# Kernel optimization log

Hardware: AMD Instinct MI355X
Metric: run time of the kernel (lower is better)

The kernel has to match this reference:

```python
import jax, jax.numpy as jnp
import numpy as np

B, I, H = 8192, 1024, 1024

def setup_inputs() -> dict:
    key = jax.random.key(0)
    ks = jax.random.split(key, 5)
    # xavier-uniform-ish scale for weights
    sW = float(np.sqrt(6.0 / (I + H)))
    sU = float(np.sqrt(6.0 / (H + H)))
    return {
        "x": jax.random.normal(ks[0], (B, I), jnp.float32),
        "h": jax.random.normal(ks[1], (B, H), jnp.float32),
        "c": jax.random.normal(ks[2], (B, H), jnp.float32),
        # gate order along leading axis: 0=i, 1=f, 2=o, 3=c_hat
        "W": jax.random.uniform(ks[3], (4, H, I), jnp.float32, -sW, sW),
        "bW": jnp.zeros((4, H), jnp.float32),
        "U": jax.random.uniform(ks[4], (4, H, H), jnp.float32, -sU, sU),
        "bU": jnp.zeros((4, H), jnp.float32),
    }

def reference(x, h, c, W, bW, U, bU):
    # two batched GEMMs covering all 8 original Linear layers
    gx = jnp.einsum('bi,ghi->gbh', x, W) + bW[:, None, :]   # [4,B,H]
    gh = jnp.einsum('bk,ghk->gbh', h, U) + bU[:, None, :]   # [4,B,H]
    g = gx + gh
    i = jax.nn.sigmoid(g[0])
    f = jax.nn.sigmoid(g[1])
    o = jax.nn.sigmoid(g[2])
    c_hat = jnp.tanh(g[3])
    c_new = f * c + i * c_hat
    h_new = o * jnp.tanh(c_new)
    return (h_new, (h_new, c_new))
```

## Files before the change

kernel.cpp:

```cpp
#include <hip/hip_runtime.h>
#include <hip/hip_bf16.h>

typedef __hip_bfloat16 bf16;
typedef __attribute__((ext_vector_type(8))) short short8;
typedef __attribute__((ext_vector_type(4))) float floatx4;

#define B_DIM 8192
#define H_DIM 1024
#define KSUM 2048
#define BM 128
#define BN 128
#define BK 64
#define KITER 32
#define CEX_STRIDE 68

union BS { bf16 b; short s; };
__device__ __forceinline__ short cvt1(float f) {
  BS u; u.b = __float2bfloat16(f); return u.s;
}
__device__ __forceinline__ short8 cvt8(float4 lo, float4 hi) {
  short8 r;
  r[0] = cvt1(lo.x); r[1] = cvt1(lo.y); r[2] = cvt1(lo.z); r[3] = cvt1(lo.w);
  r[4] = cvt1(hi.x); r[5] = cvt1(hi.y); r[6] = cvt1(hi.z); r[7] = cvt1(hi.w);
  return r;
}

__device__ __forceinline__ void async_ld16(const bf16* g, bf16* lds) {
  __builtin_amdgcn_global_load_lds(
      (const __attribute__((address_space(1))) unsigned int*)g,
      (__attribute__((address_space(3))) unsigned int*)lds,
      16, 0, 0);
}

__global__ __launch_bounds__(256) void cvt_pack(
    const float* __restrict__ x, const float* __restrict__ h,
    const float* __restrict__ W, const float* __restrict__ U,
    bf16* __restrict__ Ac, bf16* __restrict__ Bc) {
  const int blk = blockIdx.x;
  if (blk < 8192) {
    const int idx = blk * 256 + threadIdx.x;
    const long row = idx >> 8;
    const int k0 = (idx & 255) << 3;
    const float* src = (k0 < 1024) ? (x + row * 1024 + k0)
                                   : (h + row * 1024 + (k0 - 1024));
    const float4 lo = *(const float4*)src;
    const float4 hi = *(const float4*)(src + 4);
    *(short8*)(Ac + row * KSUM + k0) = cvt8(lo, hi);
  } else {
    const int idx = (blk - 8192) * 256 + threadIdx.x;
    const long r = idx >> 8;
    const int k0 = (idx & 255) << 3;
    const int g = (int)(r & 3);
    const long hh = r >> 2;
    const long base = (long)g * (H_DIM * H_DIM) + hh * H_DIM;
    const float* src = (k0 < 1024) ? (W + base + k0) : (U + base + (k0 - 1024));
    const float4 lo = *(const float4*)src;
    const float4 hi = *(const float4*)(src + 4);
    *(short8*)(Bc + r * KSUM + k0) = cvt8(lo, hi);
  }
}

__device__ __forceinline__ float sigmoidf_(float v) {
  return 1.0f / (1.0f + __expf(-v));
}
__device__ __forceinline__ float tanhf_(float v) {
  return 1.0f - 2.0f / (__expf(2.0f * v) + 1.0f);
}
__device__ __forceinline__ float getc(const float4& v, int t) {
  return t == 0 ? v.x : t == 1 ? v.y : t == 2 ? v.z : v.w;
}

__global__ __launch_bounds__(256) void gemm_lstm(
    const bf16* __restrict__ Ac, const bf16* __restrict__ Bc,
    const float* __restrict__ cprev_g, const float* __restrict__ bW,
    const float* __restrict__ bU, float* __restrict__ out) {
  __shared__ __align__(16) char smem[65536];
  bf16* const sA0 = (bf16*)smem;
  bf16* const sB0 = (bf16*)(smem + 16384);
  bf16* const sA1 = (bf16*)(smem + 32768);
  bf16* const sB1 = (bf16*)(smem + 49152);
  float* const cex = (float*)smem;

  const int tid  = threadIdx.x;
  const int lane = tid & 63;
  const int wv   = tid >> 6;

  const int blk  = blockIdx.x;
  const int xcd  = blk & 7;
  const int slot = blk >> 3;
  const int mt   = slot & 63;
  const int nt   = (xcd << 2) | (slot >> 6);
  const long m0 = (long)mt * BM;
  const long n0 = (long)nt * BN;

  const int lrow   = lane >> 3;
  const int lchunk = lane & 7;
  const int schunk = lchunk ^ lrow;
  const bf16* aSrc = Ac + (m0 + wv * 8 + lrow) * (long)KSUM + schunk * 8;
  const bf16* bSrc = Bc + (n0 + wv * 8 + lrow) * (long)KSUM + schunk * 8;
  bf16* const dA0 = sA0 + wv * 512;
  bf16* const dB0 = sB0 + wv * 512;
  bf16* const dA1 = sA1 + wv * 512;
  bf16* const dB1 = sB1 + wv * 512;

  const int wm = ((wv >> 1) & 1) << 6;
  const int wn = (wv & 1) << 6;
  const int col16 = lane & 15;
  const int quad  = lane >> 4;
  const int x7    = col16 & 7;

  floatx4 acc[4][4];
#pragma unroll
  for (int i = 0; i < 4; ++i)
#pragma unroll
    for (int j = 0; j < 4; ++j) acc[i][j] = (floatx4){0.f, 0.f, 0.f, 0.f};

#define STAGE(kt, dA, dB)                                                 \
  {                                                                       \
    const long koff_ = (long)(kt) * BK;                                   \
    _Pragma("unroll")                                                     \
    for (int q = 0; q < 4; ++q) {                                         \
      async_ld16(aSrc + koff_ + (long)q * (32 * (long)KSUM), (dA) + q * 2048); \
      async_ld16(bSrc + koff_ + (long)q * (32 * (long)KSUM), (dB) + q * 2048); \
    }                                                                     \
  }

#define COMPUTE(sAp, sBp)                                                 \
  {                                                                       \
    _Pragma("unroll")                                                     \
    for (int s = 0; s < 2; ++s) {                                         \
      const int cp = ((((s << 2) + quad) ^ x7) << 3);                     \
      short8 af[4], bfr[4];                                               \
      _Pragma("unroll")                                                   \
      for (int i = 0; i < 4; ++i) {                                       \
        af[i]  = *(const short8*)&(sAp)[(wm + i * 16 + col16) * 64 + cp]; \
        bfr[i] = *(const short8*)&(sBp)[(wn + i * 16 + col16) * 64 + cp]; \
      }                                                                   \
      _Pragma("unroll")                                                   \
      for (int i = 0; i < 4; ++i)                                         \
        _Pragma("unroll")                                                 \
        for (int j = 0; j < 4; ++j)                                       \
          acc[i][j] = __builtin_amdgcn_mfma_f32_16x16x32_bf16(            \
              af[i], bfr[j], acc[i][j], 0, 0, 0);                         \
    }                                                                     \
  }

  STAGE(0, dA0, dB0);
#pragma unroll 1
  for (int kt = 0; kt < KITER; kt += 2) {
    __syncthreads();
    STAGE(kt + 1, dA1, dB1);
    COMPUTE(sA0, sB0);
    __syncthreads();
    if (kt + 2 < KITER) STAGE(kt + 2, dA0, dB0);
    COMPUTE(sA1, sB1);
  }

  __syncthreads();

  const int rquad = (lane >> 4) << 2;
  const int row16 = lane & 15;
  const int tq    = lane >> 4;
  const long hglob = (n0 >> 2) + (wn >> 2) + tq * 4;

  float4 bsum[4];
#pragma unroll
  for (int g = 0; g < 4; ++g) {
    const float4 a = *(const float4*)(bW + g * H_DIM + hglob);
    const float4 b = *(const float4*)(bU + g * H_DIM + hglob);
    bsum[g] = (float4){a.x + b.x, a.y + b.y, a.z + b.z, a.w + b.w};
  }

  float* wx = cex + wv * (16 * CEX_STRIDE);
  const long BH = (long)B_DIM * H_DIM;

  for (int ig = 0; ig < 4; ++ig) {
#pragma unroll
    for (int j = 0; j < 4; ++j)
#pragma unroll
      for (int r = 0; r < 4; ++r)
        wx[(rquad + r) * CEX_STRIDE + j * 16 + col16] = acc[ig][j][r];

    float4 g4[4];
#pragma unroll
    for (int t = 0; t < 4; ++t)
      g4[t] = *(const float4*)&wx[row16 * CEX_STRIDE + (tq * 4 + t) * 4];

    const long mrow = m0 + wm + ig * 16 + row16;
    const float4 cp4 = *(const float4*)(cprev_g + mrow * H_DIM + hglob);

    float hn[4], cn[4];
#pragma unroll
    for (int t = 0; t < 4; ++t) {
      const float gi = g4[t].x + getc(bsum[0], t);
      const float gf = g4[t].y + getc(bsum[1], t);
      const float go = g4[t].z + getc(bsum[2], t);
      const float gg = g4[t].w + getc(bsum[3], t);
      const float I = sigmoidf_(gi);
      const float F = sigmoidf_(gf);
      const float O = sigmoidf_(go);
      const float G = tanhf_(gg);
      const float cv = F * getc(cp4, t) + I * G;
      hn[t] = O * tanhf_(cv);
      cn[t] = cv;
    }
    const float4 hn4 = {hn[0], hn[1], hn[2], hn[3]};
    const float4 cn4 = {cn[0], cn[1], cn[2], cn[3]};
    const long ob = mrow * H_DIM + hglob;
    *(float4*)(out + ob)          = hn4;
    *(float4*)(out + BH + ob)     = hn4;
    *(float4*)(out + 2 * BH + ob) = cn4;
  }
}

extern "C" void kernel_launch(void* const* d_in, const int* in_sizes, int n_in,
                              void* d_out, int out_size, void* d_ws, size_t ws_size,
                              hipStream_t stream) {
  const float* x  = (const float*)d_in[0];
  const float* h  = (const float*)d_in[1];
  const float* c  = (const float*)d_in[2];
  const float* W  = (const float*)d_in[3];
  const float* bW = (const float*)d_in[4];
  const float* U  = (const float*)d_in[5];
  const float* bU = (const float*)d_in[6];
  float* out = (float*)d_out;

  bf16* Ac = (bf16*)d_ws;
  bf16* Bc = (bf16*)((char*)d_ws + (size_t)33554432);

  cvt_pack<<<12288, 256, 0, stream>>>(x, h, W, U, Ac, Bc);
  gemm_lstm<<<2048, 256, 0, stream>>>(Ac, Bc, c, bW, bU, out);
}
```

Before: 374.7 us.

## Use 256x256 tiles with 8 waves and a 10-slot async LDS ring pipeline

Grows the GEMM tile from 128x128 to 256x256 with 512 threads per block, so each block reuses more of A and B per LDS load. Global-to-LDS loads are issued in half-tile chunks into a 10-slot ring buffer, so several stages stay in flight while MFMAs run. The main loop is split into four quarter phases that interleave LDS reads, prefetches, barriers and MFMA bursts, with setprio raising the priority of the MFMA bursts. The cost is 160 KB of dynamic LDS and many more accumulator registers per wave, which limits occupancy, plus more barriers per K step.

```diff
diff --git a/kernel.cpp b/kernel.cpp
--- a/kernel.cpp
+++ b/kernel.cpp
@@ -8,10 +8,12 @@
 #define B_DIM 8192
 #define H_DIM 1024
 #define KSUM 2048
-#define BM 128
-#define BN 128
+#define BM 256
+#define BN 256
 #define BK 64
-#define KITER 32
+#define KT 32
+#define NSLOT 10
+#define SLOT_ELEMS 8192
 #define CEX_STRIDE 68
 
 union BS { bf16 b; short s; };
@@ -70,98 +72,115 @@
   return t == 0 ? v.x : t == 1 ? v.y : t == 2 ? v.z : v.w;
 }
 
-__global__ __launch_bounds__(256) void gemm_lstm(
+__global__ __launch_bounds__(512, 2) void gemm_lstm(
     const bf16* __restrict__ Ac, const bf16* __restrict__ Bc,
     const float* __restrict__ cprev_g, const float* __restrict__ bW,
     const float* __restrict__ bU, float* __restrict__ out) {
-  __shared__ __align__(16) char smem[65536];
-  bf16* const sA0 = (bf16*)smem;
-  bf16* const sB0 = (bf16*)(smem + 16384);
-  bf16* const sA1 = (bf16*)(smem + 32768);
-  bf16* const sB1 = (bf16*)(smem + 49152);
+  extern __shared__ __align__(16) char smem[];
+  bf16* const ring = (bf16*)smem;
   float* const cex = (float*)smem;
 
   const int tid  = threadIdx.x;
   const int lane = tid & 63;
   const int wv   = tid >> 6;
+  const int wm_idx = wv >> 2;
+  const int wn_idx = wv & 3;
 
   const int blk  = blockIdx.x;
   const int xcd  = blk & 7;
   const int slot = blk >> 3;
-  const int mt   = slot & 63;
-  const int nt   = (xcd << 2) | (slot >> 6);
+  const int mt   = slot & 31;
+  const int nt   = (xcd << 1) | (slot >> 5);
   const long m0 = (long)mt * BM;
   const long n0 = (long)nt * BN;
 
   const int lrow   = lane >> 3;
   const int lchunk = lane & 7;
   const int schunk = lchunk ^ lrow;
-  const bf16* aSrc = Ac + (m0 + wv * 8 + lrow) * (long)KSUM + schunk * 8;
-  const bf16* bSrc = Bc + (n0 + wv * 8 + lrow) * (long)KSUM + schunk * 8;
-  bf16* const dA0 = sA0 + wv * 512;
-  bf16* const dB0 = sB0 + wv * 512;
-  bf16* const dA1 = sA1 + wv * 512;
-  bf16* const dB1 = sB1 + wv * 512;
-
-  const int wm = ((wv >> 1) & 1) << 6;
-  const int wn = (wv & 1) << 6;
+  const bf16* const aRow0 = Ac + (m0 + wv * 8 + lrow) * (long)KSUM + schunk * 8;
+  const bf16* const bRow0 = Bc + (n0 + wv * 8 + lrow) * (long)KSUM + schunk * 8;
+
   const int col16 = lane & 15;
   const int quad  = lane >> 4;
   const int x7    = col16 & 7;
-
-  floatx4 acc[4][4];
-#pragma unroll
-  for (int i = 0; i < 4; ++i)
-#pragma unroll
-    for (int j = 0; j < 4; ++j) acc[i][j] = (floatx4){0.f, 0.f, 0.f, 0.f};
-
-#define STAGE(kt, dA, dB)                                                 \
-  {                                                                       \
-    const long koff_ = (long)(kt) * BK;                                   \
-    _Pragma("unroll")                                                     \
-    for (int q = 0; q < 4; ++q) {                                         \
-      async_ld16(aSrc + koff_ + (long)q * (32 * (long)KSUM), (dA) + q * 2048); \
-      async_ld16(bSrc + koff_ + (long)q * (32 * (long)KSUM), (dB) + q * 2048); \
-    }                                                                     \
-  }
-
-#define COMPUTE(sAp, sBp)                                                 \
-  {                                                                       \
-    _Pragma("unroll")                                                     \
-    for (int s = 0; s < 2; ++s) {                                         \
-      const int cp = ((((s << 2) + quad) ^ x7) << 3);                     \
-      short8 af[4], bfr[4];                                               \
-      _Pragma("unroll")                                                   \
-      for (int i = 0; i < 4; ++i) {                                       \
-        af[i]  = *(const short8*)&(sAp)[(wm + i * 16 + col16) * 64 + cp]; \
-        bfr[i] = *(const short8*)&(sBp)[(wn + i * 16 + col16) * 64 + cp]; \
-      }                                                                   \
-      _Pragma("unroll")                                                   \
-      for (int i = 0; i < 4; ++i)                                         \
-        _Pragma("unroll")                                                 \
-        for (int j = 0; j < 4; ++j)                                       \
-          acc[i][j] = __builtin_amdgcn_mfma_f32_16x16x32_bf16(            \
-              af[i], bfr[j], acc[i][j], 0, 0, 0);                         \
-    }                                                                     \
-  }
-
-  STAGE(0, dA0, dB0);
+  const int bRowOff = (wn_idx & 1) << 6;
+
+  floatx4 acc[8][4];
+#pragma unroll
+  for (int i = 0; i < 8; ++i)
+#pragma unroll
+    for (int jq = 0; jq < 4; ++jq) acc[i][jq] = (floatx4){0.f, 0.f, 0.f, 0.f};
+
+#define STAGE_HALF(h_)                                                        \
+  {                                                                           \
+    const int c_ = (h_) & 3;                                                  \
+    const long off_ = ((long)((c_ >> 1) * 128)) * KSUM + (long)(((h_) >> 2) * BK); \
+    const bf16* s_ = ((c_ & 1) ? bRow0 : aRow0) + off_;                       \
+    bf16* d_ = ring + ((h_) % NSLOT) * SLOT_ELEMS + wv * 512;                 \
+    async_ld16(s_, d_);                                                       \
+    async_ld16(s_ + 64L * KSUM, d_ + 4096);                                   \
+  }
+
+#define READ_AF(rh_)                                                          \
+  _Pragma("unroll") for (int fi = 0; fi < 4; ++fi)                            \
+    _Pragma("unroll") for (int s = 0; s < 2; ++s)                             \
+      af_[fi][s] = *(const short8*)&rA[((rh_) * 64 + fi * 16 + col16) * 64 +  \
+                                       ((((s << 2) + quad) ^ x7) << 3)];
+
+#define READ_BF(nh_)                                                          \
+  _Pragma("unroll") for (int fj = 0; fj < 2; ++fj)                            \
+    _Pragma("unroll") for (int s = 0; s < 2; ++s)                             \
+      bf_[fj][s] = *(const short8*)&rB[(bRowOff + (nh_) * 32 + fj * 16 + col16) * 64 + \
+                                       ((((s << 2) + quad) ^ x7) << 3)];
+
+#define STAGE_P(p_)                                                           \
+  { const int h_ = 4 * j + (p_) + 6; if (h_ < 4 * KT) STAGE_HALF(h_); }
+
+#define SYNC_MID()                                                            \
+  __builtin_amdgcn_s_barrier();                                               \
+  asm volatile("s_waitcnt lgkmcnt(0)" ::: "memory");                          \
+  __builtin_amdgcn_sched_barrier(0);
+
+#define MFMA_Q(rh_, nh_)                                                      \
+  __builtin_amdgcn_s_setprio(1);                                              \
+  _Pragma("unroll") for (int fi = 0; fi < 4; ++fi)                            \
+    _Pragma("unroll") for (int fj = 0; fj < 2; ++fj)                          \
+      _Pragma("unroll") for (int s = 0; s < 2; ++s)                           \
+        acc[(rh_) * 4 + fi][(nh_) * 2 + fj] =                                 \
+            __builtin_amdgcn_mfma_f32_16x16x32_bf16(                          \
+                af_[fi][s], bf_[fj][s], acc[(rh_) * 4 + fi][(nh_) * 2 + fj],  \
+                0, 0, 0);                                                     \
+  __builtin_amdgcn_s_setprio(0);
+
+#pragma unroll
+  for (int h = 0; h < 6; ++h) STAGE_HALF(h);
+  asm volatile("s_waitcnt vmcnt(4)" ::: "memory");
+  __builtin_amdgcn_s_barrier();
+
 #pragma unroll 1
-  for (int kt = 0; kt < KITER; kt += 2) {
-    __syncthreads();
-    STAGE(kt + 1, dA1, dB1);
-    COMPUTE(sA0, sB0);
-    __syncthreads();
-    if (kt + 2 < KITER) STAGE(kt + 2, dA0, dB0);
-    COMPUTE(sA1, sB1);
-  }
-
-  __syncthreads();
+  for (int j = 0; j < KT; ++j) {
+    const bf16* const rA =
+        ring + ((4 * j + 2 * wm_idx) % NSLOT) * SLOT_ELEMS;
+    const bf16* const rB =
+        ring + ((4 * j + 1 + ((wn_idx >> 1) << 1)) % NSLOT) * SLOT_ELEMS;
+    short8 af_[4][2], bf_[2][2];
+
+    READ_AF(0) READ_BF(0) STAGE_P(0) SYNC_MID() MFMA_Q(0, 0)
+    __builtin_amdgcn_s_barrier();
+    READ_BF(1) STAGE_P(1) SYNC_MID() MFMA_Q(0, 1)
+    __builtin_amdgcn_s_barrier();
+    READ_AF(1) READ_BF(0) STAGE_P(2) SYNC_MID() MFMA_Q(1, 0)
+    __builtin_amdgcn_s_barrier();
+    READ_BF(1) STAGE_P(3) SYNC_MID() MFMA_Q(1, 1)
+    if (j < KT - 2) asm volatile("s_waitcnt vmcnt(4)" ::: "memory");
+    else            asm volatile("s_waitcnt vmcnt(0)" ::: "memory");
+    __builtin_amdgcn_s_barrier();
+  }
 
   const int rquad = (lane >> 4) << 2;
   const int row16 = lane & 15;
   const int tq    = lane >> 4;
-  const long hglob = (n0 >> 2) + (wn >> 2) + tq * 4;
+  const long hglob = ((n0 + (long)(wn_idx << 6)) >> 2) + tq * 4;
 
   float4 bsum[4];
 #pragma unroll
@@ -174,19 +193,20 @@
   float* wx = cex + wv * (16 * CEX_STRIDE);
   const long BH = (long)B_DIM * H_DIM;
 
-  for (int ig = 0; ig < 4; ++ig) {
-#pragma unroll
-    for (int j = 0; j < 4; ++j)
+#pragma unroll
+  for (int ig = 0; ig < 8; ++ig) {
+#pragma unroll
+    for (int jj = 0; jj < 4; ++jj)
 #pragma unroll
       for (int r = 0; r < 4; ++r)
-        wx[(rquad + r) * CEX_STRIDE + j * 16 + col16] = acc[ig][j][r];
+        wx[(rquad + r) * CEX_STRIDE + jj * 16 + col16] = acc[ig][jj][r];
 
     float4 g4[4];
 #pragma unroll
     for (int t = 0; t < 4; ++t)
       g4[t] = *(const float4*)&wx[row16 * CEX_STRIDE + (tq * 4 + t) * 4];
 
-    const long mrow = m0 + wm + ig * 16 + row16;
+    const long mrow = m0 + (long)wm_idx * 128 + ig * 16 + row16;
     const float4 cp4 = *(const float4*)(cprev_g + mrow * H_DIM + hglob);
 
     float hn[4], cn[4];
@@ -228,6 +248,13 @@
   bf16* Ac = (bf16*)d_ws;
   bf16* Bc = (bf16*)((char*)d_ws + (size_t)33554432);
 
+  static bool attr_done = false;
+  if (!attr_done) {
+    hipFuncSetAttribute(reinterpret_cast<const void*>(gemm_lstm),
+                        hipFuncAttributeMaxDynamicSharedMemorySize, 163840);
+    attr_done = true;
+  }
+
   cvt_pack<<<12288, 256, 0, stream>>>(x, h, W, U, Ac, Bc);
-  gemm_lstm<<<2048, 256, 0, stream>>>(Ac, Bc, c, bW, bU, out);
-}
+  gemm_lstm<<<512, 512, 163840, stream>>>(Ac, Bc, c, bW, bU, out);
+}
```

Result: faster. 348.9 us (-6.9%).
